# Kernel tuning notes

Hardware: AMD Instinct MI355X
Metric: run time of the kernel (lower is better)

Reference implementation:

```python
import jax, jax.numpy as jnp
import numpy as np

E_NUM, R_NUM, DIM = 100000, 16, 32
BATCH, MAX_STEP, NEIGH, RULES = 1024, 2, 16, 8


def setup_inputs() -> dict:
    key = jax.random.key(0)
    ks = jax.random.split(key, 8)
    users = jax.random.randint(ks[0], (BATCH,), 0, E_NUM)
    items = jax.random.randint(ks[1], (BATCH,), 0, E_NUM)
    rules = jax.random.randint(ks[2], (RULES, MAX_STEP), 0, R_NUM)
    adj = jax.random.randint(ks[3], (R_NUM + 1, E_NUM, NEIGH), 0, E_NUM).astype(jnp.int32)
    ent_embed = jax.random.normal(ks[4], (E_NUM, DIM), jnp.float32) * 0.1
    rule_w = jax.random.normal(ks[5], (RULES,), jnp.float32) * 0.5
    W = jax.random.normal(ks[6], (DIM, 2 * DIM), jnp.float32) * (1.0 / np.sqrt(2 * DIM))
    b = jnp.zeros((DIM,), jnp.float32)
    return dict(users=users, items=items, rules=rules, adj=adj,
                ent_embed=ent_embed, rule_w=rule_w, W=W, b=b)


def _renorm(v, eps=1e-7):
    # emulate nn.Embedding(max_norm=1.0): clip row norms to <= 1 at lookup time
    n = jnp.linalg.norm(v, axis=-1, keepdims=True)
    return v * jnp.minimum(1.0, 1.0 / jnp.maximum(n, eps))


def reference(users, items, rules, adj, ent_embed, rule_w, W, b):
    B = users.shape[0]
    R, S = rules.shape
    N = adj.shape[2]
    dim = ent_embed.shape[1]

    # --- gather entity ids per hop: hop k has [B, R, N^k] (rule-major, as np.hstack) ---
    cur = jnp.broadcast_to(users[:, None], (B, R)).reshape(B, R, 1)
    hops = [cur.reshape(B, -1)]
    for s in range(S):
        rid = rules[:, s]                       # [R] relation id per rule at this step
        nxt = adj[rid[None, :, None], cur]      # [B, R, K, N]
        cur = nxt.reshape(B, R, -1)
        hops.append(cur.reshape(B, -1))

    # --- embed + max_norm renorm ---
    vecs = [_renorm(ent_embed[h]) for h in hops]  # hop k: [B, R*N^k, dim]

    # --- concat aggregator across hops (dropout p=0) ---
    for i in range(S):
        act = jnp.tanh if i == S - 1 else jax.nn.relu
        nxt_vecs = []
        for hop in range(S - i):
            selfv = vecs[hop]                                # [B, M, dim]
            neigh = vecs[hop + 1].reshape(B, -1, N, dim)     # [B, M, N, dim]
            h = jnp.concatenate([selfv, neigh.mean(axis=2)], axis=-1)  # [B, M, 2*dim]
            nxt_vecs.append(act(jnp.einsum('bmd,od->bmo', h, W) + b))
        vecs = nxt_vecs

    res = vecs[0].reshape(B, R, dim)             # per-rule user representation
    rw = _renorm(rule_w[None, :])[0]             # rule_embed with max_norm=1.0
    user_out = jnp.sum(res * rw[None, :, None], axis=1)      # [B, dim]
    item_emb = _renorm(ent_embed[items])                     # [B, dim]
    return jax.nn.sigmoid(jnp.sum(user_out * item_emb, axis=-1))  # [B]
```

## Files before the change

### kernel.cpp

```cpp
#include <hip/hip_runtime.h>
#include <hip/hip_fp16.h>
#include <math.h>

#define E_NUMC 100000
#define DIMC 32
#define NEIGHC 16
#define RULESC 8

struct __align__(16) h2x4 { __half2 x, y, z, w; };
struct __align__(8)  h2x2 { __half2 x, y; };

typedef _Float16 half8 __attribute__((ext_vector_type(8)));
typedef float    floatx4 __attribute__((ext_vector_type(4)));
typedef float    fx2 __attribute__((ext_vector_type(2)));

__global__ __launch_bounds__(256) void renorm_kernel(
    const float* __restrict__ emb, short* __restrict__ o8,
    const float* __restrict__ W, _Float16* __restrict__ Whg)
{
    if (blockIdx.x == 0) {
        const float4* W4 = (const float4*)W;
        const int o = threadIdx.x >> 3, oct = threadIdx.x & 7;
        const float4 wa = W4[o * 16 + 2 * oct];
        const float4 wb = W4[o * 16 + 2 * oct + 1];
        half8 hw;
        hw[0] = (_Float16)wa.x; hw[1] = (_Float16)wa.y;
        hw[2] = (_Float16)wa.z; hw[3] = (_Float16)wa.w;
        hw[4] = (_Float16)wb.x; hw[5] = (_Float16)wb.y;
        hw[6] = (_Float16)wb.z; hw[7] = (_Float16)wb.w;
        *(half8*)&Whg[o * 64 + 8 * oct] = hw;
    }
    const int row = blockIdx.x * 16 + (threadIdx.x >> 4);
    const int j = threadIdx.x & 15;
    const float2 f = ((const float2*)(emb + (long)row * DIMC))[j];
    float sq = f.x * f.x + f.y * f.y;
    sq += __shfl_xor(sq, 1, 64);
    sq += __shfl_xor(sq, 2, 64);
    sq += __shfl_xor(sq, 4, 64);
    sq += __shfl_xor(sq, 8, 64);
    const float s = fminf(1.0f, 1.0f / fmaxf(sqrtf(sq), 1e-7f));
    const int pk = __builtin_amdgcn_cvt_pk_fp8_f32(f.x * s, f.y * s, 0, false);
    o8[(long)row * (DIMC / 2) + j] = (short)(pk & 0xffff);
}

__global__ __launch_bounds__(256, 6) void rgrec_tree16_kernel(
    const int* __restrict__ users, const int* __restrict__ rules,
    const int* __restrict__ adj, const float* __restrict__ emb,
    const uint2* __restrict__ emb8, const _Float16* __restrict__ Whg,
    const float* __restrict__ bvec, float* __restrict__ res)
{
    const int b = blockIdx.x;
    const int r = blockIdx.y;
    const int t = threadIdx.x;
    const int lane = t & 63;
    const int wave = t >> 6;

    __shared__ _Float16 Xh[16][72];
    __shared__ _Float16 Wh[32][72];
    __shared__ _Float16 u16[72];
    __shared__ float mean1p[2][36];
    __shared__ float xe[68];
    __shared__ float bs[32];

    const int user = users[b];
    const int rid0 = rules[r * 2 + 0];
    const int rid1 = rules[r * 2 + 1];

    int h1v = 0;
    if (lane < 16) h1v = adj[(rid0 * E_NUMC + user) * NEIGHC + lane];

    const int m = t >> 4;
    const int j = t & 15;
    const int e1 = __shfl(h1v, m, 64);
    const int e2 = adj[(rid1 * E_NUMC + e1) * NEIGHC + j];

    const int g = t >> 3, k8 = t & 7;
    const bool cact = (t < 136);
    float4 craw = make_float4(0.f, 0.f, 0.f, 0.f);
    if (cact) {
        const int ec = (g < 16) ? __shfl(h1v, g, 64) : user;
        craw = ((const float4*)(emb + (long)ec * DIMC))[k8];
    }

    {
        const int o = t >> 3, oct = t & 7;
        *(half8*)&Wh[o][8 * oct] = *(const half8*)&Whg[o * 64 + 8 * oct];
    }
    if (t < 32) bs[t] = bvec[t];

    {
        const int k = j & 3;
        const int h = j >> 2;
        const int gbase = t & 48;
        float acc[8];
#pragma unroll
        for (int d = 0; d < 8; ++d) acc[d] = 0.0f;
#pragma unroll
        for (int i = 0; i < 4; ++i) {
            const int ec = __shfl(e2, gbase + h + 4 * i, 64);
            const uint2 v = emb8[(long)ec * 4 + k];
            const fx2 p0 = __builtin_amdgcn_cvt_pk_f32_fp8(v.x, false);
            const fx2 p1 = __builtin_amdgcn_cvt_pk_f32_fp8(v.x, true);
            const fx2 p2 = __builtin_amdgcn_cvt_pk_f32_fp8(v.y, false);
            const fx2 p3 = __builtin_amdgcn_cvt_pk_f32_fp8(v.y, true);
            acc[0] += p0[0]; acc[1] += p0[1];
            acc[2] += p1[0]; acc[3] += p1[1];
            acc[4] += p2[0]; acc[5] += p2[1];
            acc[6] += p3[0]; acc[7] += p3[1];
        }
#pragma unroll
        for (int d = 0; d < 8; ++d) acc[d] += __shfl_xor(acc[d], 4, 64);
#pragma unroll
        for (int d = 0; d < 8; ++d) acc[d] += __shfl_xor(acc[d], 8, 64);
        *(__half2*)&Xh[m][32 + 8 * k + 2 * h] =
            __floats2half2_rn(acc[2 * h] * (1.0f / 16.0f),
                              acc[2 * h + 1] * (1.0f / 16.0f));
    }

    if (cact) {
        float sq = craw.x * craw.x + craw.y * craw.y +
                   craw.z * craw.z + craw.w * craw.w;
        sq += __shfl_xor(sq, 1, 64);
        sq += __shfl_xor(sq, 2, 64);
        sq += __shfl_xor(sq, 4, 64);
        const float s = fminf(1.0f, 1.0f / fmaxf(sqrtf(sq), 1e-7f));
        const float c0 = craw.x * s, c1 = craw.y * s;
        const float c2 = craw.z * s, c3 = craw.w * s;
        const __half2 ha = __floats2half2_rn(c0, c1);
        const __half2 hb = __floats2half2_rn(c2, c3);
        if (g < 16) {
            *(__half2*)&Xh[g][4 * k8]     = ha;
            *(__half2*)&Xh[g][4 * k8 + 2] = hb;
        } else {
            *(__half2*)&u16[4 * k8]     = ha;
            *(__half2*)&u16[4 * k8 + 2] = hb;
        }
        if (t < 128) {
            float d0 = c0, d1 = c1, d2 = c2, d3 = c3;
#pragma unroll
            for (int st = 8; st <= 32; st <<= 1) {
                d0 += __shfl_xor(d0, st, 64);
                d1 += __shfl_xor(d1, st, 64);
                d2 += __shfl_xor(d2, st, 64);
                d3 += __shfl_xor(d3, st, 64);
            }
            if ((lane & 56) == 0)
                *(float4*)&mean1p[wave][4 * k8] = make_float4(d0, d1, d2, d3);
        }
    }
    __syncthreads();

    const int cn = lane & 15;
    const int kg = lane >> 4;
    if (wave < 2) {
        const half8 a0 = *(const half8*)&Xh[cn][8 * kg];
        const half8 a1 = *(const half8*)&Xh[cn][32 + 8 * kg];
        const half8 b0 = *(const half8*)&Wh[cn + 16 * wave][8 * kg];
        const half8 b1 = *(const half8*)&Wh[cn + 16 * wave][32 + 8 * kg];
        floatx4 acc = {0.0f, 0.0f, 0.0f, 0.0f};
        acc = __builtin_amdgcn_mfma_f32_16x16x32_f16(a0, b0, acc, 0, 0, 0);
        acc = __builtin_amdgcn_mfma_f32_16x16x32_f16(a1, b1, acc, 0, 0, 0);
        const float bb = bs[cn + 16 * wave];
        float csum = 0.0f;
#pragma unroll
        for (int q = 0; q < 4; ++q) csum += fmaxf(acc[q] + bb, 0.0f);
        csum += __shfl_xor(csum, 16, 64);
        csum += __shfl_xor(csum, 32, 64);
        if (lane < 16) xe[32 + cn + 16 * wave] = csum * (1.0f / 16.0f);
    } else if (wave == 2) {
        const int o = lane & 31, h = lane >> 5;
        float a = 0.0f;
        if (h == 0) {
#pragma unroll
            for (int oct = 0; oct < 4; ++oct) {
                const half8 u = *(const half8*)&u16[8 * oct];
                const half8 w = *(const half8*)&Wh[o][8 * oct];
#pragma unroll
                for (int q = 0; q < 8; ++q) a += (float)u[q] * (float)w[q];
            }
        } else {
#pragma unroll
            for (int oct = 0; oct < 4; ++oct) {
                const half8 w = *(const half8*)&Wh[o][32 + 8 * oct];
                const float4 p0a = *(const float4*)&mean1p[0][8 * oct];
                const float4 p0b = *(const float4*)&mean1p[0][8 * oct + 4];
                const float4 p1a = *(const float4*)&mean1p[1][8 * oct];
                const float4 p1b = *(const float4*)&mean1p[1][8 * oct + 4];
                a += (float)w[0] * (p0a.x + p1a.x) + (float)w[1] * (p0a.y + p1a.y)
                   + (float)w[2] * (p0a.z + p1a.z) + (float)w[3] * (p0a.w + p1a.w)
                   + (float)w[4] * (p0b.x + p1b.x) + (float)w[5] * (p0b.y + p1b.y)
                   + (float)w[6] * (p0b.z + p1b.z) + (float)w[7] * (p0b.w + p1b.w);
            }
            a *= (1.0f / 16.0f);
        }
        a += __shfl_xor(a, 32, 64);
        if (h == 0) xe[o] = fmaxf(a + bs[o], 0.0f);
    }
    __syncthreads();

    if (t < 64) {
        const int o = lane & 31, h = lane >> 5;
        float a = 0.0f;
#pragma unroll
        for (int oct = 4 * h; oct < 4 * h + 4; ++oct) {
            const half8 w = *(const half8*)&Wh[o][8 * oct];
            const float4 xa = *(const float4*)&xe[8 * oct];
            const float4 xb = *(const float4*)&xe[8 * oct + 4];
            a += (float)w[0] * xa.x + (float)w[1] * xa.y
               + (float)w[2] * xa.z + (float)w[3] * xa.w
               + (float)w[4] * xb.x + (float)w[5] * xb.y
               + (float)w[6] * xb.z + (float)w[7] * xb.w;
        }
        a += __shfl_xor(a, 32, 64);
        if (h == 0)
            res[(b * RULESC + r) * DIMC + o] = tanhf(a + bs[o]);
    }
}

__global__ __launch_bounds__(256) void rgrec_combine_kernel(
    const int* __restrict__ items, const float* __restrict__ emb,
    const float* __restrict__ rule_w, const float* __restrict__ res,
    float* __restrict__ out, int B)
{
    const int gw = (blockIdx.x * 256 + threadIdx.x) >> 6;
    const int lane = threadIdx.x & 63;
    if (gw >= B) return;
    const int b = gw;

    float ss = 0.0f;
#pragma unroll
    for (int i = 0; i < RULESC; ++i) { const float w = rule_w[i]; ss += w * w; }
    const float rws = fminf(1.0f, 1.0f / fmaxf(sqrtf(ss), 1e-7f));

    const int d = lane & 31, rh = lane >> 5;
    float acc = 0.0f;
#pragma unroll
    for (int rr = 0; rr < 4; ++rr) {
        const int r = rh * 4 + rr;
        acc += rule_w[r] * res[(b * RULESC + r) * DIMC + d];
    }
    acc += __shfl_xor(acc, 32, 64);
    acc *= rws;

    const int it = items[b];
    const float x = emb[(long)it * DIMC + d];
    float sq = x * x;
    sq += __shfl_xor(sq, 1, 64);
    sq += __shfl_xor(sq, 2, 64);
    sq += __shfl_xor(sq, 4, 64);
    sq += __shfl_xor(sq, 8, 64);
    sq += __shfl_xor(sq, 16, 64);
    const float s = fminf(1.0f, 1.0f / fmaxf(sqrtf(sq), 1e-7f));
    float p = acc * x * s;
    p += __shfl_xor(p, 1, 64);
    p += __shfl_xor(p, 2, 64);
    p += __shfl_xor(p, 4, 64);
    p += __shfl_xor(p, 8, 64);
    p += __shfl_xor(p, 16, 64);
    if (lane == 0) out[b] = 1.0f / (1.0f + expf(-p));
}

__global__ __launch_bounds__(256) void rgrec_fused_kernel(
    const int* __restrict__ users, const int* __restrict__ items,
    const int* __restrict__ rules, const int* __restrict__ adj,
    const float* __restrict__ emb, const float* __restrict__ rule_w,
    const float* __restrict__ W, const float* __restrict__ bvec,
    float* __restrict__ out)
{
    const int b = blockIdx.x;
    const int t = threadIdx.x;

    __shared__ float Wt[64][33];
    __shared__ float bs[32];
    __shared__ float h1s[16][33];
    __shared__ float mean2[16][33];
    __shared__ float v1[16][33];
    __shared__ float u_vec[32];
    __shared__ float mean1[32];
    __shared__ float v0[32];
    __shared__ float meanv1[32];
    __shared__ float useru[32];
    __shared__ int   h1id[16];

    for (int i = t; i < 64 * 32; i += 256) {
        const int o = i >> 6, d = i & 63;
        Wt[d][o] = W[i];
    }
    if (t < 32) { bs[t] = bvec[t]; useru[t] = 0.0f; }

    float ss = 0.0f;
#pragma unroll
    for (int i = 0; i < RULESC; ++i) { const float w = rule_w[i]; ss += w * w; }
    const float rws = fminf(1.0f, 1.0f / fmaxf(sqrtf(ss), 1e-7f));

    const int user = users[b];

    for (int r = 0; r < RULESC; ++r) {
        const int rid0 = rules[r * 2 + 0];
        const int rid1 = rules[r * 2 + 1];
        if (t < 16) h1id[t] = adj[(rid0 * E_NUMC + user) * NEIGHC + t];
        __syncthreads();
        {
            const int m = t >> 4, j = t & 15;
            const int e1 = h1id[m];
            const int e2 = adj[(rid1 * E_NUMC + e1) * NEIGHC + j];
            float v[32];
            const float4* p = (const float4*)(emb + (long)e2 * DIMC);
            float sq = 0.0f;
#pragma unroll
            for (int q = 0; q < 8; ++q) {
                const float4 f = p[q];
                v[q * 4 + 0] = f.x; v[q * 4 + 1] = f.y;
                v[q * 4 + 2] = f.z; v[q * 4 + 3] = f.w;
                sq += f.x * f.x + f.y * f.y + f.z * f.z + f.w * f.w;
            }
            const float s =
                fminf(1.0f, 1.0f / fmaxf(sqrtf(sq), 1e-7f)) * (1.0f / 16.0f);
#pragma unroll
            for (int d = 0; d < 32; ++d) v[d] *= s;
#pragma unroll
            for (int st = 1; st < 16; st <<= 1) {
#pragma unroll
                for (int d = 0; d < 32; ++d) v[d] += __shfl_xor(v[d], st, 64);
            }
            mean2[m][j]      = v[j];
            mean2[m][j + 16] = v[j + 16];
        }
        if (t < 136) {
            const int g = t >> 3, k = t & 7;
            const int e = (g < 16) ? h1id[g] : user;
            const float4 f = ((const float4*)(emb + (long)e * DIMC))[k];
            float sq = f.x * f.x + f.y * f.y + f.z * f.z + f.w * f.w;
            sq += __shfl_xor(sq, 1, 64);
            sq += __shfl_xor(sq, 2, 64);
            sq += __shfl_xor(sq, 4, 64);
            const float s = fminf(1.0f, 1.0f / fmaxf(sqrtf(sq), 1e-7f));
            if (g < 16) {
                h1s[g][k * 4 + 0] = f.x * s; h1s[g][k * 4 + 1] = f.y * s;
                h1s[g][k * 4 + 2] = f.z * s; h1s[g][k * 4 + 3] = f.w * s;
            } else {
                u_vec[k * 4 + 0] = f.x * s; u_vec[k * 4 + 1] = f.y * s;
                u_vec[k * 4 + 2] = f.z * s; u_vec[k * 4 + 3] = f.w * s;
            }
        }
        __syncthreads();
        {
            const int m = t >> 4, o = t & 15;
            float a0 = bs[o], a1 = bs[o + 16];
#pragma unroll
            for (int d = 0; d < 32; ++d) {
                const float h = h1s[m][d];
                a0 += Wt[d][o] * h;
                a1 += Wt[d][o + 16] * h;
            }
#pragma unroll
            for (int d = 0; d < 32; ++d) {
                const float h = mean2[m][d];
                a0 += Wt[32 + d][o] * h;
                a1 += Wt[32 + d][o + 16] * h;
            }
            v1[m][o]      = fmaxf(a0, 0.0f);
            v1[m][o + 16] = fmaxf(a1, 0.0f);
        }
        if (t < 32) {
            float mn = 0.0f;
#pragma unroll
            for (int m2 = 0; m2 < 16; ++m2) mn += h1s[m2][t];
            mean1[t] = mn * (1.0f / 16.0f);
        }
        __syncthreads();
        if (t < 32) {
            float a = bs[t];
#pragma unroll
            for (int d = 0; d < 32; ++d) a += Wt[d][t] * u_vec[d];
#pragma unroll
            for (int d = 0; d < 32; ++d) a += Wt[32 + d][t] * mean1[d];
            v0[t] = fmaxf(a, 0.0f);
            float mv = 0.0f;
#pragma unroll
            for (int m2 = 0; m2 < 16; ++m2) mv += v1[m2][t];
            meanv1[t] = mv * (1.0f / 16.0f);
        }
        __syncthreads();
        if (t < 32) {
            float a = bs[t];
#pragma unroll
            for (int d = 0; d < 32; ++d) a += Wt[d][t] * v0[d];
#pragma unroll
            for (int d = 0; d < 32; ++d) a += Wt[32 + d][t] * meanv1[d];
            useru[t] += rule_w[r] * rws * tanhf(a);
        }
        __syncthreads();
    }

    if (t < 32) {
        const int it = items[b];
        const float x = emb[(long)it * DIMC + t];
        float sq = x * x;
        sq += __shfl_xor(sq, 1, 64);
        sq += __shfl_xor(sq, 2, 64);
        sq += __shfl_xor(sq, 4, 64);
        sq += __shfl_xor(sq, 8, 64);
        sq += __shfl_xor(sq, 16, 64);
        const float s = fminf(1.0f, 1.0f / fmaxf(sqrtf(sq), 1e-7f));
        float p = useru[t] * x * s;
        p += __shfl_xor(p, 1, 64);
        p += __shfl_xor(p, 2, 64);
        p += __shfl_xor(p, 4, 64);
        p += __shfl_xor(p, 8, 64);
        p += __shfl_xor(p, 16, 64);
        if (t == 0) out[b] = 1.0f / (1.0f + expf(-p));
    }
}

extern "C" void kernel_launch(void* const* d_in, const int* in_sizes, int n_in,
                              void* d_out, int out_size, void* d_ws, size_t ws_size,
                              hipStream_t stream) {
    const int*   users  = (const int*)d_in[0];
    const int*   items  = (const int*)d_in[1];
    const int*   rules  = (const int*)d_in[2];
    const int*   adj    = (const int*)d_in[3];
    const float* emb    = (const float*)d_in[4];
    const float* rule_w = (const float*)d_in[5];
    const float* W      = (const float*)d_in[6];
    const float* bvec   = (const float*)d_in[7];
    float*       out    = (float*)d_out;

    const int batch = in_sizes[0];
    const size_t emb8_bytes = (size_t)E_NUMC * DIMC;
    const size_t whg_bytes  = (size_t)DIMC * 2 * DIMC * sizeof(short);
    const size_t res_bytes  = (size_t)batch * RULESC * DIMC * sizeof(float);

    if (ws_size >= emb8_bytes + whg_bytes + res_bytes) {
        short*    emb8s = (short*)d_ws;
        _Float16* whg   = (_Float16*)((char*)d_ws + emb8_bytes);
        float*    res   = (float*)((char*)d_ws + emb8_bytes + whg_bytes);

        renorm_kernel<<<dim3(E_NUMC / 16), dim3(256), 0, stream>>>(
            emb, emb8s, W, whg);
        rgrec_tree16_kernel<<<dim3(batch, RULESC), dim3(256), 0, stream>>>(
            users, rules, adj, emb, (const uint2*)emb8s, whg, bvec, res);
        const int nblk = (batch * 64 + 255) / 256;
        rgrec_combine_kernel<<<dim3(nblk), dim3(256), 0, stream>>>(
            items, emb, rule_w, res, out, batch);
    } else {
        rgrec_fused_kernel<<<dim3(batch), dim3(256), 0, stream>>>(
            users, items, rules, adj, emb, rule_w, W, bvec, out);
    }
}
```

Before: 37.85 us.

## Process four rules per block with prefetched gathers for the next rule

Each block now handles four rules for one user instead of one, so the grid shrinks from batch×8 to batch×2. Weight staging, user-embedding renorm and first-hop adjacency reads are shared across those rules. The fp8 and fp32 embedding gathers for the next rule are issued before the current rule's aggregation, overlapping memory latency with compute. The cost is fewer blocks in flight, a serial per-rule loop with barriers, and higher register pressure, which is why the occupancy hint drops from 6 to 5.

After: 44.11 us. +16.5%, slower.

```diff
diff --git a/kernel.cpp b/kernel.cpp
--- a/kernel.cpp
+++ b/kernel.cpp
@@ -43,14 +43,14 @@
     o8[(long)row * (DIMC / 2) + j] = (short)(pk & 0xffff);
 }
 
-__global__ __launch_bounds__(256, 6) void rgrec_tree16_kernel(
+__global__ __launch_bounds__(256, 5) void rgrec_tree4_kernel(
     const int* __restrict__ users, const int* __restrict__ rules,
     const int* __restrict__ adj, const float* __restrict__ emb,
     const uint2* __restrict__ emb8, const _Float16* __restrict__ Whg,
     const float* __restrict__ bvec, float* __restrict__ res)
 {
     const int b = blockIdx.x;
-    const int r = blockIdx.y;
+    const int rq = blockIdx.y;
     const int t = threadIdx.x;
     const int lane = t & 63;
     const int wave = t >> 6;
@@ -63,23 +63,19 @@
     __shared__ float bs[32];
 
     const int user = users[b];
-    const int rid0 = rules[r * 2 + 0];
-    const int rid1 = rules[r * 2 + 1];
-
-    int h1v = 0;
-    if (lane < 16) h1v = adj[(rid0 * E_NUMC + user) * NEIGHC + lane];
+
+    const int rr_l = lane >> 4, idx = lane & 15;
+    const int rid0l = rules[(4 * rq + rr_l) * 2 + 0];
+    const int h1v = adj[(rid0l * E_NUMC + user) * NEIGHC + idx];
 
     const int m = t >> 4;
     const int j = t & 15;
-    const int e1 = __shfl(h1v, m, 64);
-    const int e2 = adj[(rid1 * E_NUMC + e1) * NEIGHC + j];
-
-    const int g = t >> 3, k8 = t & 7;
-    const bool cact = (t < 136);
-    float4 craw = make_float4(0.f, 0.f, 0.f, 0.f);
-    if (cact) {
-        const int ec = (g < 16) ? __shfl(h1v, g, 64) : user;
-        craw = ((const float4*)(emb + (long)ec * DIMC))[k8];
+    int e2id[4];
+#pragma unroll
+    for (int rr = 0; rr < 4; ++rr) {
+        const int rid1 = rules[(4 * rq + rr) * 2 + 1];
+        const int e1 = __shfl(h1v, rr * 16 + m, 64);
+        e2id[rr] = adj[(rid1 * E_NUMC + e1) * NEIGHC + j];
     }
 
     {
@@ -87,55 +83,94 @@
         *(half8*)&Wh[o][8 * oct] = *(const half8*)&Whg[o * 64 + 8 * oct];
     }
     if (t < 32) bs[t] = bvec[t];
-
-    {
-        const int k = j & 3;
-        const int h = j >> 2;
-        const int gbase = t & 48;
-        float acc[8];
-#pragma unroll
-        for (int d = 0; d < 8; ++d) acc[d] = 0.0f;
-#pragma unroll
-        for (int i = 0; i < 4; ++i) {
-            const int ec = __shfl(e2, gbase + h + 4 * i, 64);
-            const uint2 v = emb8[(long)ec * 4 + k];
-            const fx2 p0 = __builtin_amdgcn_cvt_pk_f32_fp8(v.x, false);
-            const fx2 p1 = __builtin_amdgcn_cvt_pk_f32_fp8(v.x, true);
-            const fx2 p2 = __builtin_amdgcn_cvt_pk_f32_fp8(v.y, false);
-            const fx2 p3 = __builtin_amdgcn_cvt_pk_f32_fp8(v.y, true);
-            acc[0] += p0[0]; acc[1] += p0[1];
-            acc[2] += p1[0]; acc[3] += p1[1];
-            acc[4] += p2[0]; acc[5] += p2[1];
-            acc[6] += p3[0]; acc[7] += p3[1];
-        }
-#pragma unroll
-        for (int d = 0; d < 8; ++d) acc[d] += __shfl_xor(acc[d], 4, 64);
-#pragma unroll
-        for (int d = 0; d < 8; ++d) acc[d] += __shfl_xor(acc[d], 8, 64);
-        *(__half2*)&Xh[m][32 + 8 * k + 2 * h] =
-            __floats2half2_rn(acc[2 * h] * (1.0f / 16.0f),
-                              acc[2 * h + 1] * (1.0f / 16.0f));
-    }
-
-    if (cact) {
-        float sq = craw.x * craw.x + craw.y * craw.y +
-                   craw.z * craw.z + craw.w * craw.w;
+    if (t < 8) {
+        const float4 u4 = ((const float4*)(emb + (long)user * DIMC))[t];
+        float sq = u4.x * u4.x + u4.y * u4.y + u4.z * u4.z + u4.w * u4.w;
         sq += __shfl_xor(sq, 1, 64);
         sq += __shfl_xor(sq, 2, 64);
         sq += __shfl_xor(sq, 4, 64);
         const float s = fminf(1.0f, 1.0f / fmaxf(sqrtf(sq), 1e-7f));
-        const float c0 = craw.x * s, c1 = craw.y * s;
-        const float c2 = craw.z * s, c3 = craw.w * s;
-        const __half2 ha = __floats2half2_rn(c0, c1);
-        const __half2 hb = __floats2half2_rn(c2, c3);
-        if (g < 16) {
-            *(__half2*)&Xh[g][4 * k8]     = ha;
-            *(__half2*)&Xh[g][4 * k8 + 2] = hb;
-        } else {
-            *(__half2*)&u16[4 * k8]     = ha;
-            *(__half2*)&u16[4 * k8 + 2] = hb;
-        }
+        *(__half2*)&u16[4 * t]     = __floats2half2_rn(u4.x * s, u4.y * s);
+        *(__half2*)&u16[4 * t + 2] = __floats2half2_rn(u4.z * s, u4.w * s);
+    }
+
+    const int kc = j & 3;
+    const int hc = j >> 2;
+    const int gbase = t & 48;
+    const int g = t >> 3, k8 = t & 7;
+
+    uint2 vv0, vv1, vv2, vv3;
+    {
+        const int ec0 = __shfl(e2id[0], gbase + hc,      64);
+        vv0 = emb8[(long)ec0 * 4 + kc];
+        const int ec1 = __shfl(e2id[0], gbase + hc + 4,  64);
+        vv1 = emb8[(long)ec1 * 4 + kc];
+        const int ec2 = __shfl(e2id[0], gbase + hc + 8,  64);
+        vv2 = emb8[(long)ec2 * 4 + kc];
+        const int ec3 = __shfl(e2id[0], gbase + hc + 12, 64);
+        vv3 = emb8[(long)ec3 * 4 + kc];
+    }
+    float4 craw = make_float4(0.f, 0.f, 0.f, 0.f);
+    if (t < 128) {
+        const int ec = __shfl(h1v, g, 64);
+        craw = ((const float4*)(emb + (long)ec * DIMC))[k8];
+    }
+
+#pragma unroll
+    for (int rr = 0; rr < 4; ++rr) {
+        uint2 nv0, nv1, nv2, nv3;
+        float4 ncr = make_float4(0.f, 0.f, 0.f, 0.f);
+        if (rr < 3) {
+            const int ec0 = __shfl(e2id[rr + 1], gbase + hc,      64);
+            nv0 = emb8[(long)ec0 * 4 + kc];
+            const int ec1 = __shfl(e2id[rr + 1], gbase + hc + 4,  64);
+            nv1 = emb8[(long)ec1 * 4 + kc];
+            const int ec2 = __shfl(e2id[rr + 1], gbase + hc + 8,  64);
+            nv2 = emb8[(long)ec2 * 4 + kc];
+            const int ec3 = __shfl(e2id[rr + 1], gbase + hc + 12, 64);
+            nv3 = emb8[(long)ec3 * 4 + kc];
+            if (t < 128) {
+                const int ec = __shfl(h1v, (rr + 1) * 16 + g, 64);
+                ncr = ((const float4*)(emb + (long)ec * DIMC))[k8];
+            }
+        }
+
+        {
+            float acc[8];
+#pragma unroll
+            for (int d = 0; d < 8; ++d) acc[d] = 0.0f;
+            const uint2 vs[4] = {vv0, vv1, vv2, vv3};
+#pragma unroll
+            for (int i = 0; i < 4; ++i) {
+                const fx2 p0 = __builtin_amdgcn_cvt_pk_f32_fp8(vs[i].x, false);
+                const fx2 p1 = __builtin_amdgcn_cvt_pk_f32_fp8(vs[i].x, true);
+                const fx2 p2 = __builtin_amdgcn_cvt_pk_f32_fp8(vs[i].y, false);
+                const fx2 p3 = __builtin_amdgcn_cvt_pk_f32_fp8(vs[i].y, true);
+                acc[0] += p0[0]; acc[1] += p0[1];
+                acc[2] += p1[0]; acc[3] += p1[1];
+                acc[4] += p2[0]; acc[5] += p2[1];
+                acc[6] += p3[0]; acc[7] += p3[1];
+            }
+#pragma unroll
+            for (int d = 0; d < 8; ++d) acc[d] += __shfl_xor(acc[d], 4, 64);
+#pragma unroll
+            for (int d = 0; d < 8; ++d) acc[d] += __shfl_xor(acc[d], 8, 64);
+            *(__half2*)&Xh[m][32 + 8 * kc + 2 * hc] =
+                __floats2half2_rn(acc[2 * hc] * (1.0f / 16.0f),
+                                  acc[2 * hc + 1] * (1.0f / 16.0f));
+        }
+
         if (t < 128) {
+            float sq = craw.x * craw.x + craw.y * craw.y +
+                       craw.z * craw.z + craw.w * craw.w;
+            sq += __shfl_xor(sq, 1, 64);
+            sq += __shfl_xor(sq, 2, 64);
+            sq += __shfl_xor(sq, 4, 64);
+            const float s = fminf(1.0f, 1.0f / fmaxf(sqrtf(sq), 1e-7f));
+            const float c0 = craw.x * s, c1 = craw.y * s;
+            const float c2 = craw.z * s, c3 = craw.w * s;
+            *(__half2*)&Xh[g][4 * k8]     = __floats2half2_rn(c0, c1);
+            *(__half2*)&Xh[g][4 * k8 + 2] = __floats2half2_rn(c2, c3);
             float d0 = c0, d1 = c1, d2 = c2, d3 = c3;
 #pragma unroll
             for (int st = 8; st <= 32; st <<= 1) {
@@ -147,73 +182,78 @@
             if ((lane & 56) == 0)
                 *(float4*)&mean1p[wave][4 * k8] = make_float4(d0, d1, d2, d3);
         }
-    }
-    __syncthreads();
-
-    const int cn = lane & 15;
-    const int kg = lane >> 4;
-    if (wave < 2) {
-        const half8 a0 = *(const half8*)&Xh[cn][8 * kg];
-        const half8 a1 = *(const half8*)&Xh[cn][32 + 8 * kg];
-        const half8 b0 = *(const half8*)&Wh[cn + 16 * wave][8 * kg];
-        const half8 b1 = *(const half8*)&Wh[cn + 16 * wave][32 + 8 * kg];
-        floatx4 acc = {0.0f, 0.0f, 0.0f, 0.0f};
-        acc = __builtin_amdgcn_mfma_f32_16x16x32_f16(a0, b0, acc, 0, 0, 0);
-        acc = __builtin_amdgcn_mfma_f32_16x16x32_f16(a1, b1, acc, 0, 0, 0);
-        const float bb = bs[cn + 16 * wave];
-        float csum = 0.0f;
-#pragma unroll
-        for (int q = 0; q < 4; ++q) csum += fmaxf(acc[q] + bb, 0.0f);
-        csum += __shfl_xor(csum, 16, 64);
-        csum += __shfl_xor(csum, 32, 64);
-        if (lane < 16) xe[32 + cn + 16 * wave] = csum * (1.0f / 16.0f);
-    } else if (wave == 2) {
-        const int o = lane & 31, h = lane >> 5;
-        float a = 0.0f;
-        if (h == 0) {
-#pragma unroll
-            for (int oct = 0; oct < 4; ++oct) {
-                const half8 u = *(const half8*)&u16[8 * oct];
+        __syncthreads();
+
+        const int cn = lane & 15;
+        const int kg = lane >> 4;
+        if (wave < 2) {
+            const half8 a0 = *(const half8*)&Xh[cn][8 * kg];
+            const half8 a1 = *(const half8*)&Xh[cn][32 + 8 * kg];
+            const half8 b0 = *(const half8*)&Wh[cn + 16 * wave][8 * kg];
+            const half8 b1 = *(const half8*)&Wh[cn + 16 * wave][32 + 8 * kg];
+            floatx4 acc = {0.0f, 0.0f, 0.0f, 0.0f};
+            acc = __builtin_amdgcn_mfma_f32_16x16x32_f16(a0, b0, acc, 0, 0, 0);
+            acc = __builtin_amdgcn_mfma_f32_16x16x32_f16(a1, b1, acc, 0, 0, 0);
+            const float bb = bs[cn + 16 * wave];
+            float csum = 0.0f;
+#pragma unroll
+            for (int q = 0; q < 4; ++q) csum += fmaxf(acc[q] + bb, 0.0f);
+            csum += __shfl_xor(csum, 16, 64);
+            csum += __shfl_xor(csum, 32, 64);
+            if (lane < 16) xe[32 + cn + 16 * wave] = csum * (1.0f / 16.0f);
+        } else if (wave == 2) {
+            const int o = lane & 31, h = lane >> 5;
+            float a = 0.0f;
+            if (h == 0) {
+#pragma unroll
+                for (int oct = 0; oct < 4; ++oct) {
+                    const half8 u = *(const half8*)&u16[8 * oct];
+                    const half8 w = *(const half8*)&Wh[o][8 * oct];
+#pragma unroll
+                    for (int q = 0; q < 8; ++q) a += (float)u[q] * (float)w[q];
+                }
+            } else {
+#pragma unroll
+                for (int oct = 0; oct < 4; ++oct) {
+                    const half8 w = *(const half8*)&Wh[o][32 + 8 * oct];
+                    const float4 p0a = *(const float4*)&mean1p[0][8 * oct];
+                    const float4 p0b = *(const float4*)&mean1p[0][8 * oct + 4];
+                    const float4 p1a = *(const float4*)&mean1p[1][8 * oct];
+                    const float4 p1b = *(const float4*)&mean1p[1][8 * oct + 4];
+                    a += (float)w[0] * (p0a.x + p1a.x) + (float)w[1] * (p0a.y + p1a.y)
+                       + (float)w[2] * (p0a.z + p1a.z) + (float)w[3] * (p0a.w + p1a.w)
+                       + (float)w[4] * (p0b.x + p1b.x) + (float)w[5] * (p0b.y + p1b.y)
+                       + (float)w[6] * (p0b.z + p1b.z) + (float)w[7] * (p0b.w + p1b.w);
+                }
+                a *= (1.0f / 16.0f);
+            }
+            a += __shfl_xor(a, 32, 64);
+            if (h == 0) xe[o] = fmaxf(a + bs[o], 0.0f);
+        }
+        __syncthreads();
+
+        if (t < 64) {
+            const int o = lane & 31, h = lane >> 5;
+            float a = 0.0f;
+#pragma unroll
+            for (int oct = 4 * h; oct < 4 * h + 4; ++oct) {
                 const half8 w = *(const half8*)&Wh[o][8 * oct];
-#pragma unroll
-                for (int q = 0; q < 8; ++q) a += (float)u[q] * (float)w[q];
-            }
-        } else {
-#pragma unroll
-            for (int oct = 0; oct < 4; ++oct) {
-                const half8 w = *(const half8*)&Wh[o][32 + 8 * oct];
-                const float4 p0a = *(const float4*)&mean1p[0][8 * oct];
-                const float4 p0b = *(const float4*)&mean1p[0][8 * oct + 4];
-                const float4 p1a = *(const float4*)&mean1p[1][8 * oct];
-                const float4 p1b = *(const float4*)&mean1p[1][8 * oct + 4];
-                a += (float)w[0] * (p0a.x + p1a.x) + (float)w[1] * (p0a.y + p1a.y)
-                   + (float)w[2] * (p0a.z + p1a.z) + (float)w[3] * (p0a.w + p1a.w)
-                   + (float)w[4] * (p0b.x + p1b.x) + (float)w[5] * (p0b.y + p1b.y)
-                   + (float)w[6] * (p0b.z + p1b.z) + (float)w[7] * (p0b.w + p1b.w);
-            }
-            a *= (1.0f / 16.0f);
-        }
-        a += __shfl_xor(a, 32, 64);
-        if (h == 0) xe[o] = fmaxf(a + bs[o], 0.0f);
-    }
-    __syncthreads();
-
-    if (t < 64) {
-        const int o = lane & 31, h = lane >> 5;
-        float a = 0.0f;
-#pragma unroll
-        for (int oct = 4 * h; oct < 4 * h + 4; ++oct) {
-            const half8 w = *(const half8*)&Wh[o][8 * oct];
-            const float4 xa = *(const float4*)&xe[8 * oct];
-            const float4 xb = *(const float4*)&xe[8 * oct + 4];
-            a += (float)w[0] * xa.x + (float)w[1] * xa.y
-               + (float)w[2] * xa.z + (float)w[3] * xa.w
-               + (float)w[4] * xb.x + (float)w[5] * xb.y
-               + (float)w[6] * xb.z + (float)w[7] * xb.w;
-        }
-        a += __shfl_xor(a, 32, 64);
-        if (h == 0)
-            res[(b * RULESC + r) * DIMC + o] = tanhf(a + bs[o]);
+                const float4 xa = *(const float4*)&xe[8 * oct];
+                const float4 xb = *(const float4*)&xe[8 * oct + 4];
+                a += (float)w[0] * xa.x + (float)w[1] * xa.y
+                   + (float)w[2] * xa.z + (float)w[3] * xa.w
+                   + (float)w[4] * xb.x + (float)w[5] * xb.y
+                   + (float)w[6] * xb.z + (float)w[7] * xb.w;
+            }
+            a += __shfl_xor(a, 32, 64);
+            if (h == 0)
+                res[(b * RULESC + 4 * rq + rr) * DIMC + o] = tanhf(a + bs[o]);
+        }
+
+        if (rr < 3) {
+            vv0 = nv0; vv1 = nv1; vv2 = nv2; vv3 = nv3;
+            craw = ncr;
+        }
     }
 }
 
@@ -438,7 +478,7 @@
 
         renorm_kernel<<<dim3(E_NUMC / 16), dim3(256), 0, stream>>>(
             emb, emb8s, W, whg);
-        rgrec_tree16_kernel<<<dim3(batch, RULESC), dim3(256), 0, stream>>>(
+        rgrec_tree4_kernel<<<dim3(batch, 2), dim3(256), 0, stream>>>(
             users, rules, adj, emb, (const uint2*)emb8s, whg, bvec, res);
         const int nblk = (batch * 64 + 255) / 256;
         rgrec_combine_kernel<<<dim3(nblk), dim3(256), 0, stream>>>(
```
